# Optimization experiments

Measured on AMD Instinct MI355X. Metric: run time of the kernel, lower is better.

## Reference

```python
import jax, jax.numpy as jnp
import numpy as np

N_SCALES = 3
BASE_SIGMA = 0.1
SCALES = jnp.asarray([BASE_SIGMA * 2.0 ** i for i in range(N_SCALES)], dtype=jnp.float32)


def setup_inputs() -> dict:
    key = jax.random.key(0)
    k_x, k_pos, k_tp, k_w1, k_b1, k_w2, k_b2 = jax.random.split(key, 7)
    B, C, T = 16, 306, 4000
    M = 128
    x = jax.random.normal(k_x, (B, C, T), dtype=jnp.float32)
    positions = jax.random.normal(k_pos, (B, C, 2), dtype=jnp.float32)
    target_positions = jax.random.normal(k_tp, (M, 2), dtype=jnp.float32)
    # nn.Linear(3, 32) / nn.Linear(32, 1) params (kaiming-uniform-ish init)
    lim1 = 1.0 / np.sqrt(3.0)
    w1 = jax.random.uniform(k_w1, (3, 32), jnp.float32, -lim1, lim1)
    b1 = jax.random.uniform(k_b1, (32,), jnp.float32, -lim1, lim1)
    lim2 = 1.0 / np.sqrt(32.0)
    w2 = jax.random.uniform(k_w2, (32, 1), jnp.float32, -lim2, lim2)
    b2 = jax.random.uniform(k_b2, (1,), jnp.float32, -lim2, lim2)
    return {"x": x, "positions": positions, "target_positions": target_positions,
            "w1": w1, "b1": b1, "w2": w2, "b2": b2}


def reference(x, positions, target_positions, w1, b1, w2, b2):
    # squared euclidean distances [B, C, M]
    diff = positions[:, :, None, :] - target_positions[None, None, :, :]
    d2 = jnp.sum(diff * diff, axis=-1)
    # multi-scale Gaussian kernels, stacked on last axis -> [B, C, M, n_scales]
    inv = 1.0 / (2.0 * SCALES ** 2)  # [n_scales]
    scale_weights = jnp.exp(-d2[..., None] * inv)
    # tiny 2-layer MLP gate: (3 -> 32 -> 1)
    h = jax.nn.relu(scale_weights @ w1 + b1)  # [B, C, M, 32]
    w = (h @ w2 + b2)[..., 0]                 # [B, C, M]
    # normalize over channel dim
    w = w / (jnp.sum(w, axis=1, keepdims=True) + 1e-8)
    # weighted channel aggregation -> [B, M, T]
    return jnp.einsum('bct,bcm->bmt', x, w)
```

## Files before the change

### kernel.cpp

```cpp
#include <hip/hip_runtime.h>

#define B_ 16
#define C_ 306
#define CP_ 320
#define T_ 4000
#define M_ 128

typedef short bf16x8 __attribute__((ext_vector_type(8)));
typedef float f32x4 __attribute__((ext_vector_type(4)));

#define WF_PER_B 81920

__global__ __launch_bounds__(320)
void gate_kernel(const float* __restrict__ positions,
                 const float* __restrict__ target,
                 const float* __restrict__ w1,
                 const float* __restrict__ b1,
                 const float* __restrict__ w2,
                 const float* __restrict__ b2,
                 unsigned short* __restrict__ wf,
                 float* __restrict__ scale) {
    const int b  = blockIdx.x >> 5;
    const int mg = blockIdx.x & 31;
    const int tid = threadIdx.x;

    __shared__ float s_w1[96], s_b1[32], s_w2[32];
    __shared__ float2 s_pos[C_];
    __shared__ float s_b2;
    __shared__ float s_tgt[8];
    __shared__ float s_part[5];
    __shared__ unsigned short s_frag[40 * 72];

    if (tid < 96) s_w1[tid] = w1[tid];
    if (tid < 32) { s_b1[tid] = b1[tid]; s_w2[tid] = w2[tid]; }
    if (tid == 256) s_b2 = b2[0];
    if (tid < C_) s_pos[tid] = ((const float2*)positions)[b * C_ + tid];
    if (tid >= 312) s_tgt[tid - 312] = target[mg * 8 + (tid - 312)];
    __syncthreads();

    float px = 0.0f, py = 0.0f;
    if (tid < C_) { px = s_pos[tid].x; py = s_pos[tid].y; }

    const int chunk = tid >> 3;
    const int slot  = tid & 7;

#pragma unroll
    for (int mi = 0; mi < 4; ++mi) {
        float w = 0.0f;
        if (tid < C_) {
            const float dx = px - s_tgt[mi * 2 + 0];
            const float dy = py - s_tgt[mi * 2 + 1];
            const float d2 = dx * dx + dy * dy;
            const float s2 = __expf(-d2 * 3.125f);
            const float q  = s2 * s2;
            const float s1 = q * q;
            const float r  = s1 * s1;
            const float s0 = r * r;
            float acc = s_b2;
#pragma unroll
            for (int j = 0; j < 32; ++j) {
                float h = fmaf(s0, s_w1[j],
                          fmaf(s1, s_w1[32 + j],
                          fmaf(s2, s_w1[64 + j], s_b1[j])));
                acc = fmaf(fmaxf(h, 0.0f), s_w2[j], acc);
            }
            w = acc;
        }

        float s = w;
#pragma unroll
        for (int off = 32; off > 0; off >>= 1) s += __shfl_down(s, off, 64);
        if ((tid & 63) == 0) s_part[tid >> 6] = s;
        __syncthreads();
        if (tid == 0) {
            float tot = s_part[0] + s_part[1] + s_part[2] + s_part[3] + s_part[4];
            scale[b * M_ + mg * 4 + mi] = 1.0f / (tot + 1e-8f);
        }
        __syncthreads();

        const unsigned int u = __float_as_uint(w);
        const unsigned short h = (unsigned short)(u >> 16);
        const float lof = w - __uint_as_float(u & 0xffff0000u);
        const unsigned short l = (unsigned short)(__float_as_uint(lof) >> 16);
        s_frag[chunk * 72 + mi * 16 + 0 + slot] = h;
        s_frag[chunk * 72 + mi * 16 + 8 + slot] = l;
    }
    __syncthreads();

    {
        const int ch = tid >> 3;
        const int g  = tid & 7;
        const uint4 v = *(const uint4*)(s_frag + ch * 72 + g * 8);
        unsigned short* dst = wf + (size_t)b * WF_PER_B
                            + (size_t)ch * 2048 + mg * 64 + g * 8;
        *(uint4*)dst = v;
    }
}

__global__ __launch_bounds__(256, 3)
void merge_gemm(const float* __restrict__ x,
                const unsigned short* __restrict__ wf,
                const float* __restrict__ scale,
                float* __restrict__ out) {
    const int t0 = blockIdx.x * 128;
    const int b  = blockIdx.y;
    const int tid  = threadIdx.x;
    const int lane = tid & 63;
    const int wv   = tid >> 6;
    const int tquad = lane >> 4;
    const int tsub  = lane & 15;

    __shared__ __align__(16) unsigned int sXh[5120];
    __shared__ __align__(16) unsigned int sXl[5120];
    __shared__ __align__(16) float sScale[M_];

    if (tid < M_) sScale[tid] = scale[b * M_ + tid];

    const float* xb = x + (size_t)b * C_ * T_;
    const unsigned short* wfB = wf + (size_t)b * WF_PER_B;

    f32x4 acc[4][4];
#pragma unroll
    for (int i = 0; i < 4; ++i)
#pragma unroll
        for (int j = 0; j < 4; ++j) acc[i][j] = (f32x4){0.f, 0.f, 0.f, 0.f};

    const int mw = (wv & 1) * 64;
    const int tw = (wv >> 1) * 64;

    const int p  = tid >> 4;
    const int tq = tid & 15;

    float4 rv[8];
#pragma unroll
    for (int s = 0; s < 2; ++s) {
        const int TQ  = tq + 16 * s;
        const int tcl = min(t0 + TQ * 4, T_ - 4);
#pragma unroll
        for (int sub = 0; sub < 2; ++sub) {
            const int cp = p + 16 * sub;
            const int c  = 2 * cp;
            rv[(s * 2 + sub) * 2 + 0] =
                *(const float4*)(xb + (size_t)min(c, C_ - 1) * T_ + tcl);
            rv[(s * 2 + sub) * 2 + 1] =
                *(const float4*)(xb + (size_t)min(c + 1, C_ - 1) * T_ + tcl);
        }
    }

    for (int step = 0; step < 5; ++step) {
        __syncthreads();

#pragma unroll
        for (int s = 0; s < 2; ++s) {
            const int TQ = tq + 16 * s;
#pragma unroll
            for (int sub = 0; sub < 2; ++sub) {
                const int cp  = p + 16 * sub;
                const int run = cp >> 2;
                const int pw  = cp & 3;
                const float* fa = (const float*)&rv[(s * 2 + sub) * 2 + 0];
                const float* fb = (const float*)&rv[(s * 2 + sub) * 2 + 1];
                const int base = run * 640 + TQ * 20 + pw;
#pragma unroll
                for (int tt = 0; tt < 4; ++tt) {
                    const unsigned int ua = __float_as_uint(fa[tt]);
                    const unsigned int ub = __float_as_uint(fb[tt]);
                    const float la = fa[tt] - __uint_as_float(ua & 0xffff0000u);
                    const float lb = fb[tt] - __uint_as_float(ub & 0xffff0000u);
                    sXh[base + tt * 4] = (ua >> 16) | (ub & 0xffff0000u);
                    sXl[base + tt * 4] = (__float_as_uint(la) >> 16) |
                                         (__float_as_uint(lb) & 0xffff0000u);
                }
            }
        }
        __syncthreads();

        if (step < 4) {
            const int c0n = (step + 1) * 64;
#pragma unroll
            for (int s = 0; s < 2; ++s) {
                const int TQ  = tq + 16 * s;
                const int tcl = min(t0 + TQ * 4, T_ - 4);
#pragma unroll
                for (int sub = 0; sub < 2; ++sub) {
                    const int c = c0n + 2 * (p + 16 * sub);
                    rv[(s * 2 + sub) * 2 + 0] =
                        *(const float4*)(xb + (size_t)min(c, C_ - 1) * T_ + tcl);
                    rv[(s * 2 + sub) * 2 + 1] =
                        *(const float4*)(xb + (size_t)min(c + 1, C_ - 1) * T_ + tcl);
                }
            }
        }

#pragma unroll
        for (int ks = 0; ks < 2; ++ks) {
            const int sub64 = step * 2 + ks;
            const int runb  = ks * 4 + tquad;

            bf16x8 bh[4], bl[4];
#pragma unroll
            for (int i = 0; i < 4; ++i) {
                const int t = tw + i * 16 + tsub;
                const int a = runb * 640 + (t >> 2) * 20 + (t & 3) * 4;
                bh[i] = *(const bf16x8*)(sXh + a);
                bl[i] = *(const bf16x8*)(sXl + a);
            }
#pragma unroll
            for (int mi = 0; mi < 4; ++mi) {
                const size_t aoff = ((size_t)(sub64 * 4 + tquad) * 128
                                   + (mw + mi * 16 + tsub)) * 16;
                const bf16x8 ah = *(const bf16x8*)(wfB + aoff);
                const bf16x8 al = *(const bf16x8*)(wfB + aoff + 8);
#pragma unroll
                for (int ti = 0; ti < 4; ++ti) {
                    acc[mi][ti] = __builtin_amdgcn_mfma_f32_16x16x32_bf16(
                        ah, bh[ti], acc[mi][ti], 0, 0, 0);
                    acc[mi][ti] = __builtin_amdgcn_mfma_f32_16x16x32_bf16(
                        ah, bl[ti], acc[mi][ti], 0, 0, 0);
                    acc[mi][ti] = __builtin_amdgcn_mfma_f32_16x16x32_bf16(
                        al, bh[ti], acc[mi][ti], 0, 0, 0);
                }
            }
        }
    }

#pragma unroll
    for (int mi = 0; mi < 4; ++mi) {
        const int mbase = mw + mi * 16 + tquad * 4;
        const float4 sc = *(const float4*)(sScale + mbase);
        float* op = out + ((size_t)b * M_ + mbase) * T_;
#pragma unroll
        for (int ti = 0; ti < 4; ++ti) {
            const int tg = t0 + tw + ti * 16 + tsub;
            if (tg < T_) {
                op[(size_t)0 * T_ + tg] = acc[mi][ti][0] * sc.x;
                op[(size_t)1 * T_ + tg] = acc[mi][ti][1] * sc.y;
                op[(size_t)2 * T_ + tg] = acc[mi][ti][2] * sc.z;
                op[(size_t)3 * T_ + tg] = acc[mi][ti][3] * sc.w;
            }
        }
    }
}

extern "C" void kernel_launch(void* const* d_in, const int* in_sizes, int n_in,
                              void* d_out, int out_size, void* d_ws, size_t ws_size,
                              hipStream_t stream) {
    const float* x         = (const float*)d_in[0];
    const float* positions = (const float*)d_in[1];
    const float* target    = (const float*)d_in[2];
    const float* w1        = (const float*)d_in[3];
    const float* b1        = (const float*)d_in[4];
    const float* w2        = (const float*)d_in[5];
    const float* b2        = (const float*)d_in[6];
    float* out = (float*)d_out;

    float* scale = (float*)d_ws;
    unsigned short* wf = (unsigned short*)(scale + B_ * M_);

    gate_kernel<<<B_ * 32, 320, 0, stream>>>(positions, target, w1, b1, w2, b2,
                                             wf, scale);

    dim3 grid((T_ + 127) / 128, B_);
    merge_gemm<<<grid, 256, 0, stream>>>(x, wf, scale, out);
}
```

Before: 150.5 us.

## Double-buffer x staging in merge GEMM with 512 threads, batch gate reductions

After: 148.4 us. No clear change (-1.4%).

```diff
diff --git a/kernel.cpp b/kernel.cpp
--- a/kernel.cpp
+++ b/kernel.cpp
@@ -2,7 +2,6 @@
 
 #define B_ 16
 #define C_ 306
-#define CP_ 320
 #define T_ 4000
 #define M_ 128
 
@@ -25,25 +24,24 @@
     const int tid = threadIdx.x;
 
     __shared__ float s_w1[96], s_b1[32], s_w2[32];
-    __shared__ float2 s_pos[C_];
     __shared__ float s_b2;
     __shared__ float s_tgt[8];
-    __shared__ float s_part[5];
+    __shared__ float s_part[4][5];
     __shared__ unsigned short s_frag[40 * 72];
 
     if (tid < 96) s_w1[tid] = w1[tid];
     if (tid < 32) { s_b1[tid] = b1[tid]; s_w2[tid] = w2[tid]; }
     if (tid == 256) s_b2 = b2[0];
-    if (tid < C_) s_pos[tid] = ((const float2*)positions)[b * C_ + tid];
     if (tid >= 312) s_tgt[tid - 312] = target[mg * 8 + (tid - 312)];
     __syncthreads();
 
     float px = 0.0f, py = 0.0f;
-    if (tid < C_) { px = s_pos[tid].x; py = s_pos[tid].y; }
-
-    const int chunk = tid >> 3;
-    const int slot  = tid & 7;
-
+    if (tid < C_) {
+        px = positions[(b * C_ + tid) * 2 + 0];
+        py = positions[(b * C_ + tid) * 2 + 1];
+    }
+
+    float wv_[4];
 #pragma unroll
     for (int mi = 0; mi < 4; ++mi) {
         float w = 0.0f;
@@ -66,18 +64,22 @@
             }
             w = acc;
         }
-
-        float s = w;
+        wv_[mi] = w;
+    }
+
+#pragma unroll
+    for (int mi = 0; mi < 4; ++mi) {
+        float s = wv_[mi];
 #pragma unroll
         for (int off = 32; off > 0; off >>= 1) s += __shfl_down(s, off, 64);
-        if ((tid & 63) == 0) s_part[tid >> 6] = s;
-        __syncthreads();
-        if (tid == 0) {
-            float tot = s_part[0] + s_part[1] + s_part[2] + s_part[3] + s_part[4];
-            scale[b * M_ + mg * 4 + mi] = 1.0f / (tot + 1e-8f);
-        }
-        __syncthreads();
-
+        if ((tid & 63) == 0) s_part[mi][tid >> 6] = s;
+    }
+
+    const int chunk = tid >> 3;
+    const int slot  = tid & 7;
+#pragma unroll
+    for (int mi = 0; mi < 4; ++mi) {
+        const float w = wv_[mi];
         const unsigned int u = __float_as_uint(w);
         const unsigned short h = (unsigned short)(u >> 16);
         const float lof = w - __uint_as_float(u & 0xffff0000u);
@@ -86,6 +88,12 @@
         s_frag[chunk * 72 + mi * 16 + 8 + slot] = l;
     }
     __syncthreads();
+
+    if (tid < 4) {
+        float tot = s_part[tid][0] + s_part[tid][1] + s_part[tid][2]
+                  + s_part[tid][3] + s_part[tid][4];
+        scale[b * M_ + mg * 4 + tid] = 1.0f / (tot + 1e-8f);
+    }
 
     {
         const int ch = tid >> 3;
@@ -97,7 +105,7 @@
     }
 }
 
-__global__ __launch_bounds__(256, 3)
+__global__ __launch_bounds__(512, 4)
 void merge_gemm(const float* __restrict__ x,
                 const unsigned short* __restrict__ wf,
                 const float* __restrict__ scale,
@@ -110,8 +118,8 @@
     const int tquad = lane >> 4;
     const int tsub  = lane & 15;
 
-    __shared__ __align__(16) unsigned int sXh[5120];
-    __shared__ __align__(16) unsigned int sXl[5120];
+    __shared__ __align__(16) unsigned int sXh[2][2560];
+    __shared__ __align__(16) unsigned int sXl[2][2560];
     __shared__ __align__(16) float sScale[M_];
 
     if (tid < M_) sScale[tid] = scale[b * M_ + tid];
@@ -119,100 +127,70 @@
     const float* xb = x + (size_t)b * C_ * T_;
     const unsigned short* wfB = wf + (size_t)b * WF_PER_B;
 
-    f32x4 acc[4][4];
+    f32x4 acc[4][2];
 #pragma unroll
     for (int i = 0; i < 4; ++i)
 #pragma unroll
-        for (int j = 0; j < 4; ++j) acc[i][j] = (f32x4){0.f, 0.f, 0.f, 0.f};
+        for (int j = 0; j < 2; ++j) acc[i][j] = (f32x4){0.f, 0.f, 0.f, 0.f};
 
     const int mw = (wv & 1) * 64;
-    const int tw = (wv >> 1) * 64;
-
-    const int p  = tid >> 4;
-    const int tq = tid & 15;
-
-    float4 rv[8];
-#pragma unroll
-    for (int s = 0; s < 2; ++s) {
-        const int TQ  = tq + 16 * s;
-        const int tcl = min(t0 + TQ * 4, T_ - 4);
-#pragma unroll
-        for (int sub = 0; sub < 2; ++sub) {
-            const int cp = p + 16 * sub;
-            const int c  = 2 * cp;
-            rv[(s * 2 + sub) * 2 + 0] =
-                *(const float4*)(xb + (size_t)min(c, C_ - 1) * T_ + tcl);
-            rv[(s * 2 + sub) * 2 + 1] =
-                *(const float4*)(xb + (size_t)min(c + 1, C_ - 1) * T_ + tcl);
-        }
-    }
-
-    for (int step = 0; step < 5; ++step) {
+    const int tw = (wv >> 1) * 32;
+
+    const int p  = tid >> 5;
+    const int TQ = tid & 31;
+    const int run = p >> 2;
+    const int pw  = p & 3;
+    const float* xcol = xb + min(t0 + TQ * 4, T_ - 4);
+    const int lbase = run * 640 + TQ * 20 + pw;
+
+    float4 cur0 = *(const float4*)(xcol + (size_t)min(2 * p,     C_ - 1) * T_);
+    float4 cur1 = *(const float4*)(xcol + (size_t)min(2 * p + 1, C_ - 1) * T_);
+
+    for (int step = 0; step < 10; ++step) {
+        float4 nxt0, nxt1;
+        if (step < 9) {
+            const int c = (step + 1) * 32 + 2 * p;
+            nxt0 = *(const float4*)(xcol + (size_t)min(c,     C_ - 1) * T_);
+            nxt1 = *(const float4*)(xcol + (size_t)min(c + 1, C_ - 1) * T_);
+        }
+
+        {
+            unsigned int* Dh = &sXh[step & 1][0];
+            unsigned int* Dl = &sXl[step & 1][0];
+            const float* fa = (const float*)&cur0;
+            const float* fb = (const float*)&cur1;
+#pragma unroll
+            for (int tt = 0; tt < 4; ++tt) {
+                const unsigned int ua = __float_as_uint(fa[tt]);
+                const unsigned int ub = __float_as_uint(fb[tt]);
+                const float la = fa[tt] - __uint_as_float(ua & 0xffff0000u);
+                const float lb = fb[tt] - __uint_as_float(ub & 0xffff0000u);
+                Dh[lbase + tt * 4] = (ua >> 16) | (ub & 0xffff0000u);
+                Dl[lbase + tt * 4] = (__float_as_uint(la) >> 16) |
+                                     (__float_as_uint(lb) & 0xffff0000u);
+            }
+        }
         __syncthreads();
 
-#pragma unroll
-        for (int s = 0; s < 2; ++s) {
-            const int TQ = tq + 16 * s;
-#pragma unroll
-            for (int sub = 0; sub < 2; ++sub) {
-                const int cp  = p + 16 * sub;
-                const int run = cp >> 2;
-                const int pw  = cp & 3;
-                const float* fa = (const float*)&rv[(s * 2 + sub) * 2 + 0];
-                const float* fb = (const float*)&rv[(s * 2 + sub) * 2 + 1];
-                const int base = run * 640 + TQ * 20 + pw;
-#pragma unroll
-                for (int tt = 0; tt < 4; ++tt) {
-                    const unsigned int ua = __float_as_uint(fa[tt]);
-                    const unsigned int ub = __float_as_uint(fb[tt]);
-                    const float la = fa[tt] - __uint_as_float(ua & 0xffff0000u);
-                    const float lb = fb[tt] - __uint_as_float(ub & 0xffff0000u);
-                    sXh[base + tt * 4] = (ua >> 16) | (ub & 0xffff0000u);
-                    sXl[base + tt * 4] = (__float_as_uint(la) >> 16) |
-                                         (__float_as_uint(lb) & 0xffff0000u);
-                }
-            }
-        }
-        __syncthreads();
-
-        if (step < 4) {
-            const int c0n = (step + 1) * 64;
-#pragma unroll
-            for (int s = 0; s < 2; ++s) {
-                const int TQ  = tq + 16 * s;
-                const int tcl = min(t0 + TQ * 4, T_ - 4);
-#pragma unroll
-                for (int sub = 0; sub < 2; ++sub) {
-                    const int c = c0n + 2 * (p + 16 * sub);
-                    rv[(s * 2 + sub) * 2 + 0] =
-                        *(const float4*)(xb + (size_t)min(c, C_ - 1) * T_ + tcl);
-                    rv[(s * 2 + sub) * 2 + 1] =
-                        *(const float4*)(xb + (size_t)min(c + 1, C_ - 1) * T_ + tcl);
-                }
-            }
-        }
-
-#pragma unroll
-        for (int ks = 0; ks < 2; ++ks) {
-            const int sub64 = step * 2 + ks;
-            const int runb  = ks * 4 + tquad;
-
-            bf16x8 bh[4], bl[4];
-#pragma unroll
-            for (int i = 0; i < 4; ++i) {
+        {
+            const unsigned int* Sh = &sXh[step & 1][0];
+            const unsigned int* Sl = &sXl[step & 1][0];
+            bf16x8 bh[2], bl[2];
+#pragma unroll
+            for (int i = 0; i < 2; ++i) {
                 const int t = tw + i * 16 + tsub;
-                const int a = runb * 640 + (t >> 2) * 20 + (t & 3) * 4;
-                bh[i] = *(const bf16x8*)(sXh + a);
-                bl[i] = *(const bf16x8*)(sXl + a);
+                const int a = tquad * 640 + (t >> 2) * 20 + (t & 3) * 4;
+                bh[i] = *(const bf16x8*)(Sh + a);
+                bl[i] = *(const bf16x8*)(Sl + a);
             }
 #pragma unroll
             for (int mi = 0; mi < 4; ++mi) {
-                const size_t aoff = ((size_t)(sub64 * 4 + tquad) * 128
+                const size_t aoff = ((size_t)(step * 4 + tquad) * 128
                                    + (mw + mi * 16 + tsub)) * 16;
                 const bf16x8 ah = *(const bf16x8*)(wfB + aoff);
                 const bf16x8 al = *(const bf16x8*)(wfB + aoff + 8);
 #pragma unroll
-                for (int ti = 0; ti < 4; ++ti) {
+                for (int ti = 0; ti < 2; ++ti) {
                     acc[mi][ti] = __builtin_amdgcn_mfma_f32_16x16x32_bf16(
                         ah, bh[ti], acc[mi][ti], 0, 0, 0);
                     acc[mi][ti] = __builtin_amdgcn_mfma_f32_16x16x32_bf16(
@@ -222,6 +200,8 @@
                 }
             }
         }
+        cur0 = nxt0;
+        cur1 = nxt1;
     }
 
 #pragma unroll
@@ -230,7 +210,7 @@
         const float4 sc = *(const float4*)(sScale + mbase);
         float* op = out + ((size_t)b * M_ + mbase) * T_;
 #pragma unroll
-        for (int ti = 0; ti < 4; ++ti) {
+        for (int ti = 0; ti < 2; ++ti) {
             const int tg = t0 + tw + ti * 16 + tsub;
             if (tg < T_) {
                 op[(size_t)0 * T_ + tg] = acc[mi][ti][0] * sc.x;
@@ -261,5 +241,5 @@
                                              wf, scale);
 
     dim3 grid((T_ + 127) / 128, B_);
-    merge_gemm<<<grid, 256, 0, stream>>>(x, wf, scale, out);
+    merge_gemm<<<grid, 512, 0, stream>>>(x, wf, scale, out);
 }
```
